# Kernel optimization log

Hardware: AMD Instinct MI355X
Metric: run time of the kernel (lower is better)

The kernel has to match this reference:

```python
import jax, jax.numpy as jnp
import numpy as np

D_MODEL = 256; N_HEADS = 8; N_LEVELS = 4; N_POINTS = 4
D_HEAD = D_MODEL // N_HEADS


def setup_inputs() -> dict:
    key = jax.random.key(0)
    ks = jax.random.split(key, 8)
    N, Lq = 4, 4096
    shapes = np.array([4096, 2048, 1024, 512], dtype=np.int32)  # temporal lengths per level
    Len_in = int(shapes.sum())  # 7680
    start = np.concatenate([[0], np.cumsum(shapes)[:-1]]).astype(np.int32)
    HLP = N_HEADS * N_LEVELS * N_POINTS
    return {
        "query": jax.random.normal(ks[0], (N, Lq, D_MODEL), jnp.float32),
        "reference_points": jax.random.uniform(ks[1], (N, Lq, N_LEVELS, 1), jnp.float32),
        "input_flatten": jax.random.normal(ks[2], (N, Len_in, D_MODEL), jnp.float32),
        "input_spatial_shapes": jnp.asarray(shapes),
        "input_level_start_index": jnp.asarray(start),
        "W_off": jax.random.normal(ks[3], (D_MODEL, HLP), jnp.float32) * 0.01,
        "b_off": jax.random.normal(ks[4], (HLP,), jnp.float32) * 2.0,
        "W_aw": jax.random.normal(ks[5], (D_MODEL, HLP), jnp.float32) * 0.02,
        "b_aw": jnp.zeros((HLP,), jnp.float32),
        "W_v": jax.random.normal(ks[6], (D_MODEL, D_MODEL), jnp.float32) / np.sqrt(D_MODEL).astype(np.float32),
        "b_v": jnp.zeros((D_MODEL,), jnp.float32),
        "W_out": jax.random.normal(ks[7], (D_MODEL, D_MODEL), jnp.float32) / np.sqrt(D_MODEL).astype(np.float32),
        "b_out": jnp.zeros((D_MODEL,), jnp.float32),
    }


def reference(query, reference_points, input_flatten, input_spatial_shapes,
              input_level_start_index, W_off, b_off, W_aw, b_aw, W_v, b_v,
              W_out, b_out):
    N, Lq, C = query.shape
    M, L, P, Dh = N_HEADS, N_LEVELS, N_POINTS, D_HEAD
    S = input_flatten.shape[1]

    value = (input_flatten @ W_v + b_v).reshape(N, S, M, Dh)
    off = (query @ W_off + b_off).reshape(N, Lq, M, L, P)
    aw = jax.nn.softmax((query @ W_aw + b_aw).reshape(N, Lq, M, L * P), axis=-1)
    aw = aw.reshape(N, Lq, M, L, P)

    # reference_points last dim == 1 branch: loc = ref + off / T_l, in [0,1]
    T = input_spatial_shapes.astype(jnp.float32)[None, None, None, :, None]  # [1,1,1,L,1]
    loc = reference_points[:, :, None, :, None, 0] + off / T  # [N,Lq,M,L,P]

    # grid_sample(align_corners=False, padding_mode='border') along W with H=1, y=0.5:
    # pixel coord x = loc*T - 0.5, clamped to [0, T-1], then linear interp.
    x = jnp.clip(loc * T - 0.5, 0.0, T - 1.0)
    x0 = jnp.floor(x)
    w1 = x - x0                                   # frac weight for right neighbor
    i0 = x0.astype(jnp.int32)
    i1 = jnp.minimum(i0 + 1, input_spatial_shapes[None, None, None, :, None] - 1)
    base = input_level_start_index[None, None, None, :, None]
    g0 = i0 + base                                # global flattened indices [N,Lq,M,L,P]
    g1 = i1 + base

    v = value.transpose(0, 2, 1, 3)               # [N,M,S,Dh]

    def gather(idx):
        idxt = idx.transpose(0, 2, 1, 3, 4).reshape(N, M, Lq * L * P, 1)
        return jnp.take_along_axis(v, idxt, axis=2).reshape(N, M, Lq, L, P, Dh)

    s0 = gather(g0)
    s1 = gather(g1)
    w1t = w1.transpose(0, 2, 1, 3, 4)[..., None]   # [N,M,Lq,L,P,1]
    samp = s0 * (1.0 - w1t) + s1 * w1t             # [N,M,Lq,L,P,Dh]

    awt = aw.transpose(0, 2, 1, 3, 4)[..., None]
    out = (samp * awt).sum(axis=(3, 4))            # [N,M,Lq,Dh]
    out = out.transpose(0, 2, 1, 3).reshape(N, Lq, M * Dh)
    return out @ W_out + b_out
```

## Files before the change

### kernel.cpp

```cpp
#include <hip/hip_runtime.h>
#include <hip/hip_bf16.h>
#include <cstddef>
#include <cstdint>

#define D_MODEL   256
#define N_HEADS   8
#define N_LEVELS  4
#define N_POINTS  4
#define D_HEAD    32
#define HLP       128
#define NBATCH    4
#define LQ        4096
#define S_LEN     7680
#define QB        8

typedef __attribute__((ext_vector_type(8))) short  short8;
typedef __attribute__((ext_vector_type(4))) float  f32x4;
typedef __attribute__((ext_vector_type(8))) unsigned short ushort8;

__device__ __forceinline__ unsigned short f2bf(float x) {
    __hip_bfloat16 h = __float2bfloat16(x);
    return *reinterpret_cast<unsigned short*>(&h);
}
__device__ __forceinline__ float bf2f(unsigned short u) {
    unsigned int v = ((unsigned int)u) << 16;
    return *reinterpret_cast<float*>(&v);
}

__device__ __forceinline__ void gload_lds16(const void* g, void* l) {
    __builtin_amdgcn_global_load_lds(
        (const __attribute__((address_space(1))) void*)g,
        (__attribute__((address_space(3))) void*)l,
        16, 0, 0);
}

__global__ __launch_bounds__(256) void prep_kernel(
    const float* __restrict__ W_v,  const float* __restrict__ W_off,
    const float* __restrict__ W_aw, const float* __restrict__ W_out,
    const float* __restrict__ b_off, const float* __restrict__ b_aw,
    unsigned short* __restrict__ Wv_t, unsigned short* __restrict__ Wcat_t,
    unsigned short* __restrict__ Wout_t, float* __restrict__ bcat)
{
    __shared__ float t[64][65];
    const int z   = blockIdx.z;
    const int k0  = blockIdx.y * 64;
    const int n0  = blockIdx.x * 64;
    const int tid = threadIdx.x;

    const float* src; int srcN; int cs; unsigned short* dst;
    if (z == 0)      { src = W_v;   srcN = 256; cs = n0;       dst = Wv_t;  }
    else if (z == 2) { src = W_out; srcN = 256; cs = n0;       dst = Wout_t;}
    else if (n0 < 128){ src = W_off; srcN = 128; cs = n0;      dst = Wcat_t;}
    else             { src = W_aw;  srcN = 128; cs = n0 - 128; dst = Wcat_t;}

    #pragma unroll
    for (int i = 0; i < 16; ++i) {
        int idx = tid + i * 256;
        int kk = idx >> 6, nn = idx & 63;
        t[kk][nn] = src[(size_t)(k0 + kk) * srcN + cs + nn];
    }
    __syncthreads();
    #pragma unroll
    for (int i = 0; i < 16; ++i) {
        int idx = tid + i * 256;
        int nn = idx >> 6, kk = idx & 63;
        dst[(size_t)(n0 + nn) * 256 + k0 + kk] = f2bf(t[kk][nn]);
    }
    if (z == 1 && blockIdx.x == 0 && blockIdx.y == 0) {
        bcat[tid] = (tid < 128) ? b_off[tid] : b_aw[tid - 128];
    }
}

__global__ __launch_bounds__(256) void gemm_vp_kernel(
    const float* __restrict__ inflat, const float* __restrict__ query,
    const unsigned short* __restrict__ Wv_t, const unsigned short* __restrict__ Wcat_t,
    const float* __restrict__ b_v, const float* __restrict__ bcat,
    unsigned short* __restrict__ value3, float* __restrict__ P)
{
    __shared__ alignas(16) unsigned short Als[8][64][8];
    __shared__ alignas(16) unsigned short Bls[8][64][8];

    const int job = blockIdx.x;
    const bool is_val = (job < 480);
    const int jj   = is_val ? job : (job - 480);
    const int row0 = (jj >> 1) * 128;
    const int col0 = (jj & 1) * 128;
    const float* A = is_val ? inflat : query;
    const unsigned short* Bt = is_val ? Wv_t : Wcat_t;
    const float* bias = is_val ? b_v : bcat;

    const int tid  = threadIdx.x;
    const int lane = tid & 63;
    const int w    = tid >> 6;
    const int wm   = w & 1;
    const int wn   = w >> 1;
    const int lr   = lane & 15;
    const int lk   = (lane >> 4) * 8;

    f32x4 acc[4][4] = {};

    for (int kt = 0; kt < 8; ++kt) {
        const int k0 = kt * 32;
        #pragma unroll
        for (int c = 0; c < 2; ++c) {
            const int im = w * 2 + c;
            const float* ap = A + (size_t)(row0 + im * 16 + lr) * 256 + k0 + lk;
            const float4 a0 = *(const float4*)(ap);
            const float4 a1 = *(const float4*)(ap + 4);
            short8 pk;
            pk[0] = (short)f2bf(a0.x); pk[1] = (short)f2bf(a0.y);
            pk[2] = (short)f2bf(a0.z); pk[3] = (short)f2bf(a0.w);
            pk[4] = (short)f2bf(a1.x); pk[5] = (short)f2bf(a1.y);
            pk[6] = (short)f2bf(a1.z); pk[7] = (short)f2bf(a1.w);
            *(short8*)&Als[im][lane][0] = pk;
            const size_t gb = (size_t)(col0 + im * 16 + lr) * 256 + k0 + lk;
            gload_lds16(Bt + gb, &Bls[im][0][0]);
        }
        __syncthreads();

        short8 af[4], bfr[4];
        #pragma unroll
        for (int i = 0; i < 4; ++i) af[i]  = *(const short8*)&Als[wm * 4 + i][lane][0];
        #pragma unroll
        for (int j = 0; j < 4; ++j) bfr[j] = *(const short8*)&Bls[wn * 4 + j][lane][0];

        #pragma unroll
        for (int i = 0; i < 4; ++i)
            #pragma unroll
            for (int j = 0; j < 4; ++j)
                acc[i][j] = __builtin_amdgcn_mfma_f32_16x16x32_bf16(
                    af[i], bfr[j], acc[i][j], 0, 0, 0);
        __syncthreads();
    }

    const int prow = (lane >> 4) * 4;
    const int pcol = lane & 15;
    if (is_val) {
        const int n  = row0 / S_LEN;
        const int s0 = row0 - n * S_LEN;
        #pragma unroll
        for (int j = 0; j < 4; ++j) {
            const int col = col0 + wn * 64 + j * 16 + pcol;
            const float bs = bias[col];
            const int m = col >> 5, d = col & 31;
            unsigned short* dst = value3 + ((size_t)(n * 8 + m) * S_LEN + s0) * 32 + d;
            #pragma unroll
            for (int i = 0; i < 4; ++i) {
                #pragma unroll
                for (int r = 0; r < 4; ++r) {
                    const int rl = wm * 64 + i * 16 + prow + r;
                    dst[(size_t)rl * 32] = f2bf(acc[i][j][r] + bs);
                }
            }
        }
    } else {
        #pragma unroll
        for (int j = 0; j < 4; ++j) {
            const int col = col0 + wn * 64 + j * 16 + pcol;
            const float bs = bias[col];
            #pragma unroll
            for (int i = 0; i < 4; ++i) {
                #pragma unroll
                for (int r = 0; r < 4; ++r) {
                    const int row = row0 + wm * 64 + i * 16 + prow + r;
                    P[(size_t)row * 256 + col] = acc[i][j][r] + bs;
                }
            }
        }
    }
}

__global__ __launch_bounds__(256) void sample_out_kernel(
    const float* __restrict__ P, const float* __restrict__ refp,
    const int* __restrict__ shapes, const int* __restrict__ lstart,
    const unsigned short* __restrict__ value3,
    const unsigned short* __restrict__ Wout_t,
    const float* __restrict__ b_out,
    float* __restrict__ out)
{
    __shared__ int   sG0[QB][132];
    __shared__ float sW [QB][132];
    __shared__ float sA [QB][132];
    __shared__ alignas(16) unsigned short T[16][264];
    __shared__ int glim[4];

    const int b    = blockIdx.x;
    const int xcd  = b & 7;
    const int n    = xcd >> 1;
    const int half = xcd & 1;
    const int slot = b >> 3;
    const int q0   = (slot * 2 + half) * QB;
    const int nq0  = n * LQ + q0;
    const int tid  = threadIdx.x;

    if (tid < 4) glim[tid] = lstart[tid] + shapes[tid] - 1;

    #pragma unroll
    for (int it = 0; it < 4; ++it) {
        const int idx = tid + it * 256;
        const int q   = idx >> 7;
        const int j   = idx & 127;
        const int l   = (j >> 2) & 3;
        const int nq  = nq0 + q;
        const float off   = __builtin_nontemporal_load(P + (size_t)nq * 256 + j);
        const float logit = __builtin_nontemporal_load(P + (size_t)nq * 256 + 128 + j);
        const float ref   = __builtin_nontemporal_load(refp + (size_t)nq * N_LEVELS + l);
        const int   sh    = shapes[l];
        const float Tf    = (float)sh;
        float x = ref * Tf + off - 0.5f;
        x = fminf(fmaxf(x, 0.0f), Tf - 1.0f);
        const float x0 = floorf(x);
        sG0[q][j] = (int)x0 + lstart[l];
        sW [q][j] = x - x0;
        sA [q][j] = logit;
    }
    __syncthreads();

    if (tid < 64) {
        const int q = tid >> 3;
        const int m = tid & 7;
        float e[16];
        float mx = -1e30f;
        #pragma unroll
        for (int i = 0; i < 16; ++i) { e[i] = sA[q][m * 16 + i]; mx = fmaxf(mx, e[i]); }
        float s = 0.f;
        #pragma unroll
        for (int i = 0; i < 16; ++i) { e[i] = __expf(e[i] - mx); s += e[i]; }
        const float rs = 1.0f / s;
        #pragma unroll
        for (int i = 0; i < 16; ++i) sA[q][m * 16 + i] = e[i] * rs;
    }
    {
        const int zr = 8 + (tid >> 5);
        const int zc = (tid & 31) * 8;
        *(ushort8*)&T[zr][zc] = (ushort8)0;
    }
    __syncthreads();

    {
        const int q  = tid >> 5;
        const int r  = tid & 31;
        const int m  = r >> 2;
        const int ql = r & 3;
        const unsigned short* vb =
            value3 + (size_t)(n * 8 + m) * S_LEN * 32 + ql * 8;

        float acc[8] = {};
        #pragma unroll
        for (int i = 0; i < 16; ++i) {
            const int j = m * 16 + i;
            const float a  = sA[q][j];
            const float ww = sW[q][j];
            const int g0 = sG0[q][j];
            const int g1 = min(g0 + 1, glim[i >> 2]);
            const ushort8 u0 = *(const ushort8*)(vb + (size_t)g0 * 32);
            const ushort8 u1 = *(const ushort8*)(vb + (size_t)g1 * 32);
            #pragma unroll
            for (int d = 0; d < 8; ++d) {
                const float v0 = bf2f(u0[d]);
                const float v1 = bf2f(u1[d]);
                acc[d] += a * (v0 + ww * (v1 - v0));
            }
        }
        ushort8 o;
        #pragma unroll
        for (int d = 0; d < 8; ++d) o[d] = f2bf(acc[d]);
        *(ushort8*)&T[q][m * 32 + ql * 8] = o;
    }
    __syncthreads();

    {
        const int w    = tid >> 6;
        const int lane = tid & 63;
        const int lr   = lane & 15;
        const int lk   = (lane >> 4) * 8;
        f32x4 acc4[4] = {};
        for (int kt = 0; kt < 8; ++kt) {
            const short8 af = *(const short8*)&T[lr][kt * 32 + lk];
            #pragma unroll
            for (int j = 0; j < 4; ++j) {
                const int col = w * 64 + j * 16 + lr;
                const short8 bf = *(const short8*)(Wout_t + (size_t)col * 256 + kt * 32 + lk);
                acc4[j] = __builtin_amdgcn_mfma_f32_16x16x32_bf16(af, bf, acc4[j], 0, 0, 0);
            }
        }
        const int prow = (lane >> 4) * 4;
        if (prow < 8) {
            #pragma unroll
            for (int j = 0; j < 4; ++j) {
                const int col = w * 64 + j * 16 + lr;
                const float bs = b_out[col];
                #pragma unroll
                for (int r = 0; r < 4; ++r) {
                    const int row = prow + r;
                    out[(size_t)(nq0 + row) * 256 + col] = acc4[j][r] + bs;
                }
            }
        }
    }
}

extern "C" void kernel_launch(void* const* d_in, const int* in_sizes, int n_in,
                              void* d_out, int out_size, void* d_ws, size_t ws_size,
                              hipStream_t stream)
{
    const float* query  = (const float*)d_in[0];
    const float* refp   = (const float*)d_in[1];
    const float* inflat = (const float*)d_in[2];
    const int*   shapes = (const int*)d_in[3];
    const int*   lstart = (const int*)d_in[4];
    const float* W_off  = (const float*)d_in[5];
    const float* b_off  = (const float*)d_in[6];
    const float* W_aw   = (const float*)d_in[7];
    const float* b_aw   = (const float*)d_in[8];
    const float* W_v    = (const float*)d_in[9];
    const float* b_v    = (const float*)d_in[10];
    const float* W_out  = (const float*)d_in[11];
    const float* b_out  = (const float*)d_in[12];

    const int M_val = NBATCH * S_LEN;
    const int M_q   = NBATCH * LQ;

    char* p = (char*)d_ws;
    unsigned short* value3 = (unsigned short*)p; p += (size_t)M_val * D_MODEL * 2;
    float*          P      = (float*)p;          p += (size_t)M_q * 256 * 4;
    unsigned short* Wv_t   = (unsigned short*)p; p += 256 * 256 * 2;
    unsigned short* Wcat_t = (unsigned short*)p; p += 256 * 256 * 2;
    unsigned short* Wout_t = (unsigned short*)p; p += 256 * 256 * 2;
    float*          bcat   = (float*)p;          p += 256 * 4;

    prep_kernel<<<dim3(4, 4, 3), 256, 0, stream>>>(
        W_v, W_off, W_aw, W_out, b_off, b_aw, Wv_t, Wcat_t, Wout_t, bcat);
    gemm_vp_kernel<<<736, 256, 0, stream>>>(
        inflat, query, Wv_t, Wcat_t, b_v, bcat, value3, P);
    sample_out_kernel<<<2048, 256, 0, stream>>>(
        P, refp, shapes, lstart, value3, Wout_t, b_out, (float*)d_out);
}
```

Baseline: 181.3 us.

## Split sampling from output GEMM, double-buffer GEMMs with 64-row tiles

The fused sample+output-projection kernel is split in two. The sampling kernel now writes bf16 intermediates to a workspace buffer, and a new double-buffered GEMM kernel computes the output projection. The value/projection GEMM moves to 64x128 tiles with register-prefetched A and double-buffered LDS for B, which doubles the grid and removes one barrier per k-step. The softmax is folded into each sampling thread so one barrier disappears, at the cost of an extra kernel launch and an extra global round trip of the intermediate.

```diff
diff --git a/kernel.cpp b/kernel.cpp
--- a/kernel.cpp
+++ b/kernel.cpp
@@ -77,13 +77,13 @@
     const float* __restrict__ b_v, const float* __restrict__ bcat,
     unsigned short* __restrict__ value3, float* __restrict__ P)
 {
-    __shared__ alignas(16) unsigned short Als[8][64][8];
-    __shared__ alignas(16) unsigned short Bls[8][64][8];
+    __shared__ alignas(16) unsigned short Abuf[2][4][64][8];
+    __shared__ alignas(16) unsigned short Bbuf[2][8][64][8];
 
     const int job = blockIdx.x;
-    const bool is_val = (job < 480);
-    const int jj   = is_val ? job : (job - 480);
-    const int row0 = (jj >> 1) * 128;
+    const bool is_val = (job < 960);
+    const int jj   = is_val ? job : (job - 960);
+    const int row0 = (jj >> 1) * 64;
     const int col0 = (jj & 1) * 128;
     const float* A = is_val ? inflat : query;
     const unsigned short* Bt = is_val ? Wv_t : Wcat_t;
@@ -92,97 +92,93 @@
     const int tid  = threadIdx.x;
     const int lane = tid & 63;
     const int w    = tid >> 6;
-    const int wm   = w & 1;
-    const int wn   = w >> 1;
     const int lr   = lane & 15;
     const int lk   = (lane >> 4) * 8;
 
-    f32x4 acc[4][4] = {};
+    const int ar = tid >> 2;
+    const int ak = (tid & 3) * 8;
+    const int afrag = ar >> 4;
+    const int alane = ((ak >> 3) << 4) | (ar & 15);
+    const float* Arow = A + (size_t)(row0 + ar) * 256 + ak;
+    const unsigned short* Bcol = Bt + (size_t)(col0 + lr) * 256 + lk;
+
+    f32x4 acc[8] = {};
+
+    float4 pa0 = *(const float4*)(Arow);
+    float4 pa1 = *(const float4*)(Arow + 4);
+    #pragma unroll
+    for (int c = 0; c < 2; ++c) {
+        const int in = w * 2 + c;
+        gload_lds16(Bcol + (size_t)in * 16 * 256, &Bbuf[0][in][0][0]);
+    }
 
     for (int kt = 0; kt < 8; ++kt) {
-        const int k0 = kt * 32;
-        #pragma unroll
-        for (int c = 0; c < 2; ++c) {
-            const int im = w * 2 + c;
-            const float* ap = A + (size_t)(row0 + im * 16 + lr) * 256 + k0 + lk;
-            const float4 a0 = *(const float4*)(ap);
-            const float4 a1 = *(const float4*)(ap + 4);
-            short8 pk;
-            pk[0] = (short)f2bf(a0.x); pk[1] = (short)f2bf(a0.y);
-            pk[2] = (short)f2bf(a0.z); pk[3] = (short)f2bf(a0.w);
-            pk[4] = (short)f2bf(a1.x); pk[5] = (short)f2bf(a1.y);
-            pk[6] = (short)f2bf(a1.z); pk[7] = (short)f2bf(a1.w);
-            *(short8*)&Als[im][lane][0] = pk;
-            const size_t gb = (size_t)(col0 + im * 16 + lr) * 256 + k0 + lk;
-            gload_lds16(Bt + gb, &Bls[im][0][0]);
-        }
+        const int cur = kt & 1;
+        short8 pk;
+        pk[0] = (short)f2bf(pa0.x); pk[1] = (short)f2bf(pa0.y);
+        pk[2] = (short)f2bf(pa0.z); pk[3] = (short)f2bf(pa0.w);
+        pk[4] = (short)f2bf(pa1.x); pk[5] = (short)f2bf(pa1.y);
+        pk[6] = (short)f2bf(pa1.z); pk[7] = (short)f2bf(pa1.w);
+        *(short8*)&Abuf[cur][afrag][alane][0] = pk;
         __syncthreads();
 
-        short8 af[4], bfr[4];
-        #pragma unroll
-        for (int i = 0; i < 4; ++i) af[i]  = *(const short8*)&Als[wm * 4 + i][lane][0];
-        #pragma unroll
-        for (int j = 0; j < 4; ++j) bfr[j] = *(const short8*)&Bls[wn * 4 + j][lane][0];
-
-        #pragma unroll
-        for (int i = 0; i < 4; ++i)
+        if (kt < 7) {
+            const int k1 = (kt + 1) * 32;
+            pa0 = *(const float4*)(Arow + k1);
+            pa1 = *(const float4*)(Arow + k1 + 4);
             #pragma unroll
-            for (int j = 0; j < 4; ++j)
-                acc[i][j] = __builtin_amdgcn_mfma_f32_16x16x32_bf16(
-                    af[i], bfr[j], acc[i][j], 0, 0, 0);
-        __syncthreads();
+            for (int c = 0; c < 2; ++c) {
+                const int in = w * 2 + c;
+                gload_lds16(Bcol + (size_t)in * 16 * 256 + k1, &Bbuf[1 - cur][in][0][0]);
+            }
+        }
+
+        const short8 af = *(const short8*)&Abuf[cur][w][lane][0];
+        #pragma unroll
+        for (int j = 0; j < 8; ++j) {
+            const short8 bf = *(const short8*)&Bbuf[cur][j][lane][0];
+            acc[j] = __builtin_amdgcn_mfma_f32_16x16x32_bf16(af, bf, acc[j], 0, 0, 0);
+        }
     }
 
     const int prow = (lane >> 4) * 4;
     const int pcol = lane & 15;
+    const int rbase = row0 + w * 16 + prow;
     if (is_val) {
         const int n  = row0 / S_LEN;
-        const int s0 = row0 - n * S_LEN;
-        #pragma unroll
-        for (int j = 0; j < 4; ++j) {
-            const int col = col0 + wn * 64 + j * 16 + pcol;
+        const int s0 = row0 - n * S_LEN + w * 16 + prow;
+        #pragma unroll
+        for (int j = 0; j < 8; ++j) {
+            const int col = col0 + j * 16 + pcol;
             const float bs = bias[col];
             const int m = col >> 5, d = col & 31;
             unsigned short* dst = value3 + ((size_t)(n * 8 + m) * S_LEN + s0) * 32 + d;
             #pragma unroll
-            for (int i = 0; i < 4; ++i) {
-                #pragma unroll
-                for (int r = 0; r < 4; ++r) {
-                    const int rl = wm * 64 + i * 16 + prow + r;
-                    dst[(size_t)rl * 32] = f2bf(acc[i][j][r] + bs);
-                }
-            }
+            for (int r = 0; r < 4; ++r)
+                dst[(size_t)r * 32] = f2bf(acc[j][r] + bs);
         }
     } else {
         #pragma unroll
-        for (int j = 0; j < 4; ++j) {
-            const int col = col0 + wn * 64 + j * 16 + pcol;
+        for (int j = 0; j < 8; ++j) {
+            const int col = col0 + j * 16 + pcol;
             const float bs = bias[col];
             #pragma unroll
-            for (int i = 0; i < 4; ++i) {
-                #pragma unroll
-                for (int r = 0; r < 4; ++r) {
-                    const int row = row0 + wm * 64 + i * 16 + prow + r;
-                    P[(size_t)row * 256 + col] = acc[i][j][r] + bs;
-                }
-            }
-        }
-    }
-}
-
-__global__ __launch_bounds__(256) void sample_out_kernel(
+            for (int r = 0; r < 4; ++r)
+                P[(size_t)(rbase + r) * 256 + col] = acc[j][r] + bs;
+        }
+    }
+}
+
+__global__ __launch_bounds__(256) void sample_kernel(
     const float* __restrict__ P, const float* __restrict__ refp,
     const int* __restrict__ shapes, const int* __restrict__ lstart,
     const unsigned short* __restrict__ value3,
-    const unsigned short* __restrict__ Wout_t,
-    const float* __restrict__ b_out,
-    float* __restrict__ out)
-{
-    __shared__ int   sG0[QB][132];
-    __shared__ float sW [QB][132];
-    __shared__ float sA [QB][132];
-    __shared__ alignas(16) unsigned short T[16][264];
-    __shared__ int glim[4];
+    unsigned short* __restrict__ tout)
+{
+    __shared__ int   sG0[QB][130];
+    __shared__ float sW [QB][130];
+    __shared__ float sA [QB][130];
+    __shared__ int   glim[4];
 
     const int b    = blockIdx.x;
     const int xcd  = b & 7;
@@ -216,87 +212,109 @@
     }
     __syncthreads();
 
-    if (tid < 64) {
-        const int q = tid >> 3;
-        const int m = tid & 7;
-        float e[16];
-        float mx = -1e30f;
-        #pragma unroll
-        for (int i = 0; i < 16; ++i) { e[i] = sA[q][m * 16 + i]; mx = fmaxf(mx, e[i]); }
-        float s = 0.f;
-        #pragma unroll
-        for (int i = 0; i < 16; ++i) { e[i] = __expf(e[i] - mx); s += e[i]; }
-        const float rs = 1.0f / s;
-        #pragma unroll
-        for (int i = 0; i < 16; ++i) sA[q][m * 16 + i] = e[i] * rs;
-    }
-    {
-        const int zr = 8 + (tid >> 5);
-        const int zc = (tid & 31) * 8;
-        *(ushort8*)&T[zr][zc] = (ushort8)0;
-    }
-    __syncthreads();
-
-    {
-        const int q  = tid >> 5;
-        const int r  = tid & 31;
-        const int m  = r >> 2;
-        const int ql = r & 3;
-        const unsigned short* vb =
-            value3 + (size_t)(n * 8 + m) * S_LEN * 32 + ql * 8;
-
-        float acc[8] = {};
-        #pragma unroll
-        for (int i = 0; i < 16; ++i) {
-            const int j = m * 16 + i;
-            const float a  = sA[q][j];
-            const float ww = sW[q][j];
-            const int g0 = sG0[q][j];
-            const int g1 = min(g0 + 1, glim[i >> 2]);
-            const ushort8 u0 = *(const ushort8*)(vb + (size_t)g0 * 32);
-            const ushort8 u1 = *(const ushort8*)(vb + (size_t)g1 * 32);
+    const int q  = tid >> 5;
+    const int r  = tid & 31;
+    const int m  = r >> 2;
+    const int ql = r & 3;
+    const unsigned short* vb =
+        value3 + (size_t)(n * 8 + m) * S_LEN * 32 + ql * 8;
+
+    float e[16];
+    float mx = -1e30f;
+    #pragma unroll
+    for (int i = 0; i < 16; ++i) { e[i] = sA[q][m * 16 + i]; mx = fmaxf(mx, e[i]); }
+    float s = 0.f;
+    #pragma unroll
+    for (int i = 0; i < 16; ++i) { e[i] = __expf(e[i] - mx); s += e[i]; }
+    const float rs = 1.0f / s;
+
+    float acc[8] = {};
+    #pragma unroll
+    for (int i = 0; i < 16; ++i) {
+        const int j = m * 16 + i;
+        const float a  = e[i] * rs;
+        const float ww = sW[q][j];
+        const int g0 = sG0[q][j];
+        const int g1 = min(g0 + 1, glim[i >> 2]);
+        const ushort8 u0 = *(const ushort8*)(vb + (size_t)g0 * 32);
+        const ushort8 u1 = *(const ushort8*)(vb + (size_t)g1 * 32);
+        #pragma unroll
+        for (int d = 0; d < 8; ++d) {
+            const float v0 = bf2f(u0[d]);
+            const float v1 = bf2f(u1[d]);
+            acc[d] += a * (v0 + ww * (v1 - v0));
+        }
+    }
+    ushort8 o;
+    #pragma unroll
+    for (int d = 0; d < 8; ++d) o[d] = f2bf(acc[d]);
+    __builtin_nontemporal_store(o,
+        (ushort8*)(tout + (size_t)(nq0 + q) * 256 + m * 32 + ql * 8));
+}
+
+__global__ __launch_bounds__(256) void gemm_out_kernel(
+    const unsigned short* __restrict__ A,
+    const unsigned short* __restrict__ Bt,
+    const float* __restrict__ bias,
+    float* __restrict__ Cout)
+{
+    __shared__ alignas(16) unsigned short Abuf[2][4][64][8];
+    __shared__ alignas(16) unsigned short Bbuf[2][8][64][8];
+
+    const int jj   = blockIdx.x;
+    const int row0 = (jj >> 1) * 64;
+    const int col0 = (jj & 1) * 128;
+
+    const int tid  = threadIdx.x;
+    const int lane = tid & 63;
+    const int w    = tid >> 6;
+    const int lr   = lane & 15;
+    const int lk   = (lane >> 4) * 8;
+
+    const unsigned short* Arow = A + (size_t)(row0 + w * 16 + lr) * 256 + lk;
+    const unsigned short* Bcol = Bt + (size_t)(col0 + lr) * 256 + lk;
+
+    f32x4 acc[8] = {};
+
+    gload_lds16(Arow, &Abuf[0][w][0][0]);
+    #pragma unroll
+    for (int c = 0; c < 2; ++c) {
+        const int in = w * 2 + c;
+        gload_lds16(Bcol + (size_t)in * 16 * 256, &Bbuf[0][in][0][0]);
+    }
+
+    for (int kt = 0; kt < 8; ++kt) {
+        const int cur = kt & 1;
+        __syncthreads();
+
+        if (kt < 7) {
+            const int k1 = (kt + 1) * 32;
+            gload_lds16(Arow + k1, &Abuf[1 - cur][w][0][0]);
             #pragma unroll
-            for (int d = 0; d < 8; ++d) {
-                const float v0 = bf2f(u0[d]);
-                const float v1 = bf2f(u1[d]);
-                acc[d] += a * (v0 + ww * (v1 - v0));
+            for (int c = 0; c < 2; ++c) {
+                const int in = w * 2 + c;
+                gload_lds16(Bcol + (size_t)in * 16 * 256 + k1, &Bbuf[1 - cur][in][0][0]);
             }
         }
-        ushort8 o;
-        #pragma unroll
-        for (int d = 0; d < 8; ++d) o[d] = f2bf(acc[d]);
-        *(ushort8*)&T[q][m * 32 + ql * 8] = o;
-    }
-    __syncthreads();
-
-    {
-        const int w    = tid >> 6;
-        const int lane = tid & 63;
-        const int lr   = lane & 15;
-        const int lk   = (lane >> 4) * 8;
-        f32x4 acc4[4] = {};
-        for (int kt = 0; kt < 8; ++kt) {
-            const short8 af = *(const short8*)&T[lr][kt * 32 + lk];
-            #pragma unroll
-            for (int j = 0; j < 4; ++j) {
-                const int col = w * 64 + j * 16 + lr;
-                const short8 bf = *(const short8*)(Wout_t + (size_t)col * 256 + kt * 32 + lk);
-                acc4[j] = __builtin_amdgcn_mfma_f32_16x16x32_bf16(af, bf, acc4[j], 0, 0, 0);
-            }
-        }
-        const int prow = (lane >> 4) * 4;
-        if (prow < 8) {
-            #pragma unroll
-            for (int j = 0; j < 4; ++j) {
-                const int col = w * 64 + j * 16 + lr;
-                const float bs = b_out[col];
-                #pragma unroll
-                for (int r = 0; r < 4; ++r) {
-                    const int row = prow + r;
-                    out[(size_t)(nq0 + row) * 256 + col] = acc4[j][r] + bs;
-                }
-            }
-        }
+
+        const short8 af = *(const short8*)&Abuf[cur][w][lane][0];
+        #pragma unroll
+        for (int j = 0; j < 8; ++j) {
+            const short8 bf = *(const short8*)&Bbuf[cur][j][lane][0];
+            acc[j] = __builtin_amdgcn_mfma_f32_16x16x32_bf16(af, bf, acc[j], 0, 0, 0);
+        }
+    }
+
+    const int prow = (lane >> 4) * 4;
+    const int pcol = lane & 15;
+    const int rbase = row0 + w * 16 + prow;
+    #pragma unroll
+    for (int j = 0; j < 8; ++j) {
+        const int col = col0 + j * 16 + pcol;
+        const float bs = bias[col];
+        #pragma unroll
+        for (int r = 0; r < 4; ++r)
+            Cout[(size_t)(rbase + r) * 256 + col] = acc[j][r] + bs;
     }
 }
 
@@ -324,6 +342,7 @@
     char* p = (char*)d_ws;
     unsigned short* value3 = (unsigned short*)p; p += (size_t)M_val * D_MODEL * 2;
     float*          P      = (float*)p;          p += (size_t)M_q * 256 * 4;
+    unsigned short* tbuf   = (unsigned short*)p; p += (size_t)M_q * D_MODEL * 2;
     unsigned short* Wv_t   = (unsigned short*)p; p += 256 * 256 * 2;
     unsigned short* Wcat_t = (unsigned short*)p; p += 256 * 256 * 2;
     unsigned short* Wout_t = (unsigned short*)p; p += 256 * 256 * 2;
@@ -331,8 +350,10 @@
 
     prep_kernel<<<dim3(4, 4, 3), 256, 0, stream>>>(
         W_v, W_off, W_aw, W_out, b_off, b_aw, Wv_t, Wcat_t, Wout_t, bcat);
-    gemm_vp_kernel<<<736, 256, 0, stream>>>(
+    gemm_vp_kernel<<<1472, 256, 0, stream>>>(
         inflat, query, Wv_t, Wcat_t, b_v, bcat, value3, P);
-    sample_out_kernel<<<2048, 256, 0, stream>>>(
-        P, refp, shapes, lstart, value3, Wout_t, b_out, (float*)d_out);
-}
+    sample_kernel<<<2048, 256, 0, stream>>>(
+        P, refp, shapes, lstart, value3, tbuf);
+    gemm_out_kernel<<<512, 256, 0, stream>>>(
+        tbuf, Wout_t, b_out, (float*)d_out);
+}
```

Result: faster. 161.7 us (-10.8%).
